# Optimization experiments

Hardware: AMD Instinct MI355X
Metric: run time of the kernel (lower is better)

The kernel has to match this reference:

```python
import jax, jax.numpy as jnp
import numpy as np

K = 8
B = 3.0
DIM = 32
HID = 32
BATCH = 65536
MIN_BW = 1e-3
MIN_BH = 1e-3
MIN_D = 1e-3


def setup_inputs() -> dict:
    key = jax.random.key(0)
    ks = jax.random.split(key, 8)
    L = DIM - 1
    x = jax.random.normal(ks[0], (BATCH, DIM), jnp.float32)
    init_param = jax.random.uniform(ks[1], (3 * K - 1,), jnp.float32, -0.5, 0.5)
    # stacked per-dim FCNN weights; layer l conditions on x[:, :l+1] -> causal zero-mask
    w1 = jax.random.normal(ks[2], (L, L, HID), jnp.float32) * 0.2
    mask = (jnp.arange(L)[None, :] <= jnp.arange(L)[:, None]).astype(jnp.float32)
    w1 = w1 * mask[:, :, None]
    b1 = jax.random.normal(ks[3], (L, HID), jnp.float32) * 0.1
    w2 = jax.random.normal(ks[4], (L, HID, HID), jnp.float32) * 0.2
    b2 = jax.random.normal(ks[5], (L, HID), jnp.float32) * 0.1
    w3 = jax.random.normal(ks[6], (L, HID, 3 * K - 1), jnp.float32) * 0.2
    b3 = jax.random.normal(ks[7], (L, 3 * K - 1), jnp.float32) * 0.1
    return {"x": x, "init_param": init_param, "w1": w1, "b1": b1,
            "w2": w2, "b2": b2, "w3": w3, "b3": b3}


def _rqs_forward(x, Wu, Hu, Du):
    # x: [dim, batch]; Wu, Hu: [dim, batch, K]; Du: [dim, batch, K-1]
    inside = (x >= -B) & (x <= B)
    xc = jnp.clip(x, -B, B)
    # bin widths
    widths = jax.nn.softmax(Wu, axis=-1)
    widths = MIN_BW + (1.0 - MIN_BW * K) * widths
    cw = jnp.cumsum(widths, axis=-1)
    cw = jnp.concatenate([jnp.zeros(cw.shape[:-1] + (1,), cw.dtype), cw], axis=-1)
    cw = 2.0 * B * cw - B
    cw = cw.at[..., 0].set(-B).at[..., -1].set(B)
    widths = cw[..., 1:] - cw[..., :-1]
    # bin heights
    heights = jax.nn.softmax(Hu, axis=-1)
    heights = MIN_BH + (1.0 - MIN_BH * K) * heights
    ch = jnp.cumsum(heights, axis=-1)
    ch = jnp.concatenate([jnp.zeros(ch.shape[:-1] + (1,), ch.dtype), ch], axis=-1)
    ch = 2.0 * B * ch - B
    ch = ch.at[..., 0].set(-B).at[..., -1].set(B)
    heights = ch[..., 1:] - ch[..., :-1]
    # knot derivatives, edges pinned so softplus(const)+min_d = 1
    const = float(np.log(np.exp(1.0 - MIN_D) - 1.0))
    pad = jnp.full(Du.shape[:-1] + (1,), const, Du.dtype)
    derivs = MIN_D + jax.nn.softplus(jnp.concatenate([pad, Du, pad], axis=-1))  # [.., K+1]
    # bin search (searchsorted on cumwidths, eps bump on last edge)
    cw_s = cw.at[..., -1].add(1e-6)
    idx = jnp.sum((xc[..., None] >= cw_s).astype(jnp.int32), axis=-1) - 1
    idx = jnp.clip(idx, 0, K - 1)
    g = lambda a: jnp.take_along_axis(a, idx[..., None], axis=-1)[..., 0]
    in_cw = g(cw)
    in_w = g(widths)
    in_ch = g(ch)
    in_h = g(heights)
    in_delta = g(heights / widths)
    d0 = g(derivs)
    d1 = g(derivs[..., 1:])
    theta = (xc - in_cw) / in_w
    tt = theta * (1.0 - theta)
    num = in_h * (in_delta * theta ** 2 + d0 * tt)
    den = in_delta + (d0 + d1 - 2.0 * in_delta) * tt
    out = in_ch + num / den
    dnum = in_delta ** 2 * (d1 * theta ** 2 + 2.0 * in_delta * tt + d0 * (1.0 - theta) ** 2)
    ld = jnp.log(dnum) - 2.0 * jnp.log(den)
    out = jnp.where(inside, out, x)  # identity tails
    ld = jnp.where(inside, ld, 0.0)
    return out, ld


def reference(x, init_param, w1, b1, w2, b2, w3, b3):
    # all per-dim conditioners at once (w1 is causally masked in setup)
    h1 = jnp.tanh(jnp.einsum('bd,ldh->lbh', x[:, :DIM - 1], w1) + b1[:, None, :])
    h2 = jnp.tanh(jnp.einsum('lbh,lhg->lbg', h1, w2) + b2[:, None, :])
    out = jnp.einsum('lbh,lho->lbo', h2, w3) + b3[:, None, :]  # [dim-1, batch, 3K-1]
    p0 = jnp.broadcast_to(init_param, (1, x.shape[0], 3 * K - 1))
    params = jnp.concatenate([p0, out], axis=0)  # [dim, batch, 3K-1]
    Wu = 2.0 * B * jax.nn.softmax(params[..., :K], axis=-1)
    Hu = 2.0 * B * jax.nn.softmax(params[..., K:2 * K], axis=-1)
    Du = jax.nn.softplus(params[..., 2 * K:])
    z_t, ld = _rqs_forward(x.T, Wu, Hu, Du)  # [dim, batch]
    return z_t.T, jnp.sum(ld, axis=0)
```

## Files before the change

kernel.cpp:

```cpp
#include <hip/hip_runtime.h>
#include <hip/hip_bf16.h>
#include <cmath>

constexpr int KN   = 8;
constexpr int NPAR = 23;
constexpr int DD   = 32;
constexpr float BND   = 3.0f;
constexpr float MINBW = 1e-3f;
constexpr float MIND  = 1e-3f;

#define TPB   256
#define ROWS  256
#define GDIMS 4
#define WST   40
#define PSTH  28
#define RECB  8192

typedef __attribute__((ext_vector_type(8))) short short8;
typedef __attribute__((ext_vector_type(4))) float float4v;
typedef __attribute__((ext_vector_type(2))) __fp16 fp16x2;
typedef __attribute__((ext_vector_type(4))) _Float16 half4v;

#define RCP(x) __builtin_amdgcn_rcpf(x)

__device__ __forceinline__ short f2bf(float f) {
    unsigned u = __float_as_uint(f);
    u += 0x7fffu + ((u >> 16) & 1u);
    return (short)(u >> 16);
}

__device__ __forceinline__ int pkbf(float a, float b) {
    union { __hip_bfloat162 v; int i; } u;
    u.v = __float22bfloat162_rn(make_float2(a, b));
    return u.i;
}

__device__ __forceinline__ int pkh(float a, float b) {
    union { fp16x2 h; int i; } u;
    u.h = __builtin_amdgcn_cvt_pkrtz(a, b);
    return u.i;
}

__device__ __forceinline__ float fast_tanh(float x) {
    float e = __expf(2.0f * x);
    return 1.0f - 2.0f * RCP(e + 1.0f);
}

__device__ __forceinline__ float softplus_fast(float v) {
    return __logf(1.0f + __expf(v));
}

__device__ __forceinline__ float rqs_apply(float xv, const float* p, float& ldout) {
    float cw[KN + 1], ch[KN + 1];
    {
        float t0[KN]; float s = 0.f;
#pragma unroll
        for (int k = 0; k < KN; ++k) { t0[k] = __expf(p[k]); s += t0[k]; }
        float inv = (2.0f * BND) * RCP(s);
        float e2[KN]; float s2 = 0.f;
#pragma unroll
        for (int k = 0; k < KN; ++k) { e2[k] = __expf(inv * t0[k]); s2 += e2[k]; }
        float fac = (1.0f - MINBW * KN) * RCP(s2);
        float c = 0.f;
        cw[0] = -BND;
#pragma unroll
        for (int k = 0; k < KN; ++k) { c += MINBW + fac * e2[k]; cw[k + 1] = 2.0f * BND * c - BND; }
        cw[KN] = BND;
    }
    {
        float t0[KN]; float s = 0.f;
#pragma unroll
        for (int k = 0; k < KN; ++k) { t0[k] = __expf(p[KN + k]); s += t0[k]; }
        float inv = (2.0f * BND) * RCP(s);
        float e2[KN]; float s2 = 0.f;
#pragma unroll
        for (int k = 0; k < KN; ++k) { e2[k] = __expf(inv * t0[k]); s2 += e2[k]; }
        float fac = (1.0f - MINBW * KN) * RCP(s2);
        float c = 0.f;
        ch[0] = -BND;
#pragma unroll
        for (int k = 0; k < KN; ++k) { c += MINBW + fac * e2[k]; ch[k + 1] = 2.0f * BND * c - BND; }
        ch[KN] = BND;
    }

    float xc = fminf(fmaxf(xv, -BND), BND);
    float in_cw = cw[0], in_w = cw[1] - cw[0];
    float in_ch = ch[0], in_h = ch[1] - ch[0];
    float dl0 = 0.0f, dl1 = p[2 * KN];
    bool e0 = true, e1 = false;
#pragma unroll
    for (int k = 1; k < KN; ++k) {
        bool c = (xc >= cw[k]);
        in_cw = c ? cw[k]            : in_cw;
        in_w  = c ? (cw[k+1]-cw[k])  : in_w;
        in_ch = c ? ch[k]            : in_ch;
        in_h  = c ? (ch[k+1]-ch[k])  : in_h;
        dl0   = c ? p[2*KN + k - 1]  : dl0;
        if (k < KN - 1) dl1 = c ? p[2*KN + k] : dl1;
        if (k == 1)      e0 = !c;
        if (k == KN - 1) e1 = c;
    }
    float d0 = e0 ? 1.0f : (MIND + softplus_fast(softplus_fast(dl0)));
    float d1 = e1 ? 1.0f : (MIND + softplus_fast(softplus_fast(dl1)));

    float rw    = RCP(in_w);
    float th    = (xc - in_cw) * rw;
    float delta = in_h * rw;
    float tt    = th * (1.0f - th);
    float th2   = th * th;
    float num   = in_h * (delta * th2 + d0 * tt);
    float den   = delta + (d0 + d1 - 2.0f * delta) * tt;
    float z     = in_ch + num * RCP(den);
    float omt   = 1.0f - th;
    float dnum  = delta * delta * (d1 * th2 + 2.0f * delta * tt + d0 * omt * omt);
    float ldv   = __logf(dnum) - 2.0f * __logf(den);

    bool inside = (xv >= -BND) && (xv <= BND);
    ldout = inside ? ldv : 0.0f;
    return inside ? z : xv;
}

__device__ __forceinline__ short8 xpose_h(float4v cA, float4v cB,
                                          int odd, int sl_a, int sl_b, bool qlow) {
    int a0 = pkbf(fast_tanh(cA[0]), fast_tanh(cA[1]));
    int a1 = pkbf(fast_tanh(cA[2]), fast_tanh(cA[3]));
    int b0 = pkbf(fast_tanh(cB[0]), fast_tanh(cB[1]));
    int b1 = pkbf(fast_tanh(cB[2]), fast_tanh(cB[3]));
    int p0 = odd ? b0 : a0, p1 = odd ? b1 : a1;
    int p2 = odd ? a0 : b0, p3 = odd ? a1 : b1;
    int g0 = __shfl(p0, sl_a, 64);
    int g1 = __shfl(p1, sl_a, 64);
    int g2 = __shfl(p2, sl_b, 64);
    int g3 = __shfl(p3, sl_b, 64);
    union { int4 i; short8 s; } u;
    u.i = qlow ? make_int4(g0, g1, g2, g3) : make_int4(g2, g3, g0, g1);
    return u.s;
}

__device__ __forceinline__ float4v f4v(float4 v) {
    float4v r; r[0] = v.x; r[1] = v.y; r[2] = v.z; r[3] = v.w; return r;
}

struct WFrag {
    short8 w1a, w1b, w2a, w2b, w3a, w3b;
    float4v bA1, bB1, bA2, bB2, bA3, bB3;
};

__device__ __forceinline__ WFrag load_wfrag(const char* __restrict__ wbuf,
                                            int l, int ln, int q) {
    const char* rec = wbuf + (size_t)l * RECB;
    const short* rw = (const short*)rec;
    const float* rb = (const float*)(rec + 7680);
    WFrag f;
    f.w1a = *(const short8*)&rw[ln * WST + q * 8];
    f.w1b = *(const short8*)&rw[(16 + ln) * WST + q * 8];
    f.w2a = *(const short8*)&rw[1280 + ln * WST + q * 8];
    f.w2b = *(const short8*)&rw[1280 + (16 + ln) * WST + q * 8];
    f.w3a = *(const short8*)&rw[2560 + ln * WST + q * 8];
    f.w3b = *(const short8*)&rw[2560 + (16 + ln) * WST + q * 8];
    f.bA1 = f4v(*(const float4*)&rb[4 * q]);
    f.bB1 = f4v(*(const float4*)&rb[16 + 4 * q]);
    f.bA2 = f4v(*(const float4*)&rb[32 + 4 * q]);
    f.bB2 = f4v(*(const float4*)&rb[48 + 4 * q]);
    f.bA3 = f4v(*(const float4*)&rb[64 + 4 * q]);
    f.bB3 = f4v(*(const float4*)&rb[80 + 4 * q]);
    return f;
}

extern "C" __global__ void __launch_bounds__(256)
k_prep(const float* __restrict__ w1, const float* __restrict__ b1,
       const float* __restrict__ w2, const float* __restrict__ b2,
       const float* __restrict__ w3, const float* __restrict__ b3,
       char* __restrict__ wbuf, float* __restrict__ ldo, int B)
{
    const int l = blockIdx.x, tid = threadIdx.x;
    if (l >= 31) {
        const int zb = l - 31;
        const int chunk = B >> 6;
        float4* dst = (float4*)(ldo + (size_t)zb * chunk);
        for (int i = tid; i < (chunk >> 2); i += 256)
            dst[i] = make_float4(0.f, 0.f, 0.f, 0.f);
        return;
    }
    short* r1 = (short*)(wbuf + (size_t)l * RECB);
    short* r2 = r1 + 1280;
    short* r3 = r2 + 1280;
    float* f1 = (float*)(wbuf + (size_t)l * RECB + 7680);
    float* f2 = f1 + 32;
    float* f3 = f2 + 32;
    const float* g1 = w1 + (size_t)l * 992;
    const float* g2 = w2 + (size_t)l * 1024;
    const float* g3 = w3 + (size_t)l * 736;
    for (int i = tid; i < 1280; i += 256) {
        int n = i / WST, k = i - WST * n;
        r1[i] = (k < 31) ? f2bf(g1[k * 32 + n]) : (short)0;
        r2[i] = (k < 32) ? f2bf(g2[k * 32 + n]) : (short)0;
        r3[i] = (n < 23 && k < 32) ? f2bf(g3[k * 23 + n]) : (short)0;
    }
    if (tid < 32) { f1[tid] = b1[(size_t)l * 32 + tid]; f2[tid] = b2[(size_t)l * 32 + tid]; }
    if (tid < 32) f3[tid] = (tid < 23) ? b3[(size_t)l * 23 + tid] : 0.0f;
}

extern "C" __global__ void __launch_bounds__(TPB, 3)
k_nsf(const float* __restrict__ x,
      const float* __restrict__ p0,
      const char* __restrict__ wbuf,
      float* __restrict__ zo, float* __restrict__ ldo, int B)
{
    __shared__ __align__(16) _Float16 sP[ROWS * PSTH];

    const int tid  = threadIdx.x;
    const int lane = tid & 63;
    const int wv   = tid >> 6;
    const int q    = lane >> 4;
    const int ln   = lane & 15;
    const int qb   = q & 1;
    const bool qlow = (q < 2);
    const int s_even = ln + 32 * qb;
    const int s_odd  = s_even + 16;
    const int sl_a = qlow ? s_even : s_odd;
    const int sl_b = qlow ? s_odd  : s_even;
    const int g    = blockIdx.y;
    const int ly0  = GDIMS * g;
    const long long rowbase = (long long)blockIdx.x * ROWS;
    const long long row = rowbase + tid;

    float xarr[GDIMS];
    {
        float4 xs = *(const float4*)(x + row * DD + ly0);
        xarr[0] = xs.x; xarr[1] = xs.y; xarr[2] = xs.z; xarr[3] = xs.w;
    }

    short8 au[4];
#pragma unroll
    for (int t = 0; t < 4; ++t) {
        const int m0 = 64 * wv + 16 * t;
        const float4* xp = (const float4*)(x + (rowbase + m0 + ln) * DD + q * 8);
        float4 uu = xp[0], vv = xp[1];
        union { int4 i; short8 s; } c;
        c.i = make_int4(pkbf(uu.x, uu.y), pkbf(uu.z, uu.w),
                        pkbf(vv.x, vv.y), pkbf(vv.z, vv.w));
        au[t] = c.s;
    }

    float zreg[GDIMS];
    float ldacc = 0.0f;

    WFrag wf = load_wfrag(wbuf, (ly0 == 0) ? 0 : ly0 - 1, ln, q);

#pragma unroll
    for (int j = 0; j < GDIMS; ++j) {
        const int ly = ly0 + j;
        if (ly == 0) {
            float pr[NPAR];
#pragma unroll
            for (int k = 0; k < NPAR; ++k) pr[k] = p0[k];
            float ld;
            zreg[0] = rqs_apply(xarr[0], pr, ld);
            ldacc += ld;
            continue;
        }

        float4v cA[4], cB[4];
#pragma unroll
        for (int t = 0; t < 4; ++t) {
            cA[t] = __builtin_amdgcn_mfma_f32_16x16x32_bf16(wf.w1a, au[t], wf.bA1, 0, 0, 0);
            cB[t] = __builtin_amdgcn_mfma_f32_16x16x32_bf16(wf.w1b, au[t], wf.bB1, 0, 0, 0);
        }
        short8 h1f[4];
#pragma unroll
        for (int t = 0; t < 4; ++t)
            h1f[t] = xpose_h(cA[t], cB[t], qb, sl_a, sl_b, qlow);
#pragma unroll
        for (int t = 0; t < 4; ++t) {
            cA[t] = __builtin_amdgcn_mfma_f32_16x16x32_bf16(wf.w2a, h1f[t], wf.bA2, 0, 0, 0);
            cB[t] = __builtin_amdgcn_mfma_f32_16x16x32_bf16(wf.w2b, h1f[t], wf.bB2, 0, 0, 0);
        }
#pragma unroll
        for (int t = 0; t < 4; ++t)
            h1f[t] = xpose_h(cA[t], cB[t], qb, sl_a, sl_b, qlow);
#pragma unroll
        for (int t = 0; t < 4; ++t) {
            cA[t] = __builtin_amdgcn_mfma_f32_16x16x32_bf16(wf.w3a, h1f[t], wf.bA3, 0, 0, 0);
            cB[t] = __builtin_amdgcn_mfma_f32_16x16x32_bf16(wf.w3b, h1f[t], wf.bB3, 0, 0, 0);
        }
#pragma unroll
        for (int t = 0; t < 4; ++t) {
            const int m0 = 64 * wv + 16 * t;
            int2 pv0 = make_int2(pkh(cA[t][0], cA[t][1]), pkh(cA[t][2], cA[t][3]));
            *(int2*)&sP[(m0 + ln) * PSTH + 4 * q] = pv0;
            if (qlow) {
                int2 pv1 = make_int2(pkh(cB[t][0], cB[t][1]), pkh(cB[t][2], cB[t][3]));
                *(int2*)&sP[(m0 + ln) * PSTH + 16 + 4 * q] = pv1;
            }
        }

        WFrag wfn;
        if (j + 1 < GDIMS) wfn = load_wfrag(wbuf, ly, ln, q);

        {
            const _Float16* pp = &sP[tid * PSTH];
            float pr[24];
#pragma unroll
            for (int u = 0; u < 6; ++u) {
                half4v hv = *(const half4v*)(pp + 4 * u);
                pr[4*u+0] = (float)hv[0];
                pr[4*u+1] = (float)hv[1];
                pr[4*u+2] = (float)hv[2];
                pr[4*u+3] = (float)hv[3];
            }
            float ld;
            zreg[j] = rqs_apply(xarr[j], pr, ld);
            ldacc += ld;
        }
        if (j + 1 < GDIMS) wf = wfn;
    }

    float4 zv = make_float4(zreg[0], zreg[1], zreg[2], zreg[3]);
    *(float4*)(zo + row * DD + ly0) = zv;
    unsafeAtomicAdd(&ldo[row], ldacc);
}

extern "C" void kernel_launch(void* const* d_in, const int* in_sizes, int n_in,
                              void* d_out, int out_size, void* d_ws, size_t ws_size,
                              hipStream_t stream) {
    const float* x  = (const float*)d_in[0];
    const float* p0 = (const float*)d_in[1];
    const float* w1 = (const float*)d_in[2];
    const float* b1 = (const float*)d_in[3];
    const float* w2 = (const float*)d_in[4];
    const float* b2 = (const float*)d_in[5];
    const float* w3 = (const float*)d_in[6];
    const float* b3 = (const float*)d_in[7];

    const int B = in_sizes[0] / DD;
    float* zo  = (float*)d_out;
    float* ldo = zo + (size_t)B * DD;
    char* wbuf = (char*)d_ws;

    hipLaunchKernelGGL(k_prep, dim3(95), dim3(256), 0, stream,
                       w1, b1, w2, b2, w3, b3, wbuf, ldo, B);
    hipLaunchKernelGGL(k_nsf, dim3(B / ROWS, DD / GDIMS), dim3(TPB), 0, stream,
                       x, p0, wbuf, zo, ldo, B);
}
```

Before: 143.4 us.

## Double-buffer spline params in LDS to overlap next MFMA MLP with spline

Splits the per-dimension step into an MFMA conditioner phase that packs spline parameters into one of two LDS buffers, and a spline phase that reads the previous dimension's buffer. Software-pipelines the loop so the GEMMs for dimension j run before the spline for dimension j-1, letting matrix and vector work interleave. Uses explicit lgkmcnt waits instead of barriers, since each thread only reads its own row. Doubles the LDS footprint and lowers the occupancy hint from 3 to 2 blocks per CU to give more registers, at the cost of fewer resident waves for latency hiding.

```diff
diff --git a/kernel.cpp b/kernel.cpp
--- a/kernel.cpp
+++ b/kernel.cpp
@@ -16,10 +16,11 @@
 #define PSTH  28
 #define RECB  8192
 
+#define LGKM_FENCE() asm volatile("s_waitcnt lgkmcnt(0)" ::: "memory")
+
 typedef __attribute__((ext_vector_type(8))) short short8;
 typedef __attribute__((ext_vector_type(4))) float float4v;
 typedef __attribute__((ext_vector_type(2))) __fp16 fp16x2;
-typedef __attribute__((ext_vector_type(4))) _Float16 half4v;
 
 #define RCP(x) __builtin_amdgcn_rcpf(x)
 
@@ -201,13 +202,14 @@
     if (tid < 32) f3[tid] = (tid < 23) ? b3[(size_t)l * 23 + tid] : 0.0f;
 }
 
-extern "C" __global__ void __launch_bounds__(TPB, 3)
+extern "C" __global__ void __launch_bounds__(TPB, 2)
 k_nsf(const float* __restrict__ x,
       const float* __restrict__ p0,
       const char* __restrict__ wbuf,
       float* __restrict__ zo, float* __restrict__ ldo, int B)
 {
-    __shared__ __align__(16) _Float16 sP[ROWS * PSTH];
+    __shared__ __align__(16) _Float16 sPa[ROWS * PSTH];
+    __shared__ __align__(16) _Float16 sPb[ROWS * PSTH];
 
     const int tid  = threadIdx.x;
     const int lane = tid & 63;
@@ -246,75 +248,82 @@
     float zreg[GDIMS];
     float ldacc = 0.0f;
 
-    WFrag wf = load_wfrag(wbuf, (ly0 == 0) ? 0 : ly0 - 1, ln, q);
-
-#pragma unroll
-    for (int j = 0; j < GDIMS; ++j) {
-        const int ly = ly0 + j;
-        if (ly == 0) {
-            float pr[NPAR];
-#pragma unroll
-            for (int k = 0; k < NPAR; ++k) pr[k] = p0[k];
-            float ld;
-            zreg[0] = rqs_apply(xarr[0], pr, ld);
-            ldacc += ld;
-            continue;
-        }
-
+    auto gemm_pack = [&](const WFrag& wf, _Float16* buf) {
         float4v cA[4], cB[4];
 #pragma unroll
         for (int t = 0; t < 4; ++t) {
             cA[t] = __builtin_amdgcn_mfma_f32_16x16x32_bf16(wf.w1a, au[t], wf.bA1, 0, 0, 0);
             cB[t] = __builtin_amdgcn_mfma_f32_16x16x32_bf16(wf.w1b, au[t], wf.bB1, 0, 0, 0);
         }
-        short8 h1f[4];
+        short8 hf[4];
 #pragma unroll
         for (int t = 0; t < 4; ++t)
-            h1f[t] = xpose_h(cA[t], cB[t], qb, sl_a, sl_b, qlow);
+            hf[t] = xpose_h(cA[t], cB[t], qb, sl_a, sl_b, qlow);
 #pragma unroll
         for (int t = 0; t < 4; ++t) {
-            cA[t] = __builtin_amdgcn_mfma_f32_16x16x32_bf16(wf.w2a, h1f[t], wf.bA2, 0, 0, 0);
-            cB[t] = __builtin_amdgcn_mfma_f32_16x16x32_bf16(wf.w2b, h1f[t], wf.bB2, 0, 0, 0);
+            cA[t] = __builtin_amdgcn_mfma_f32_16x16x32_bf16(wf.w2a, hf[t], wf.bA2, 0, 0, 0);
+            cB[t] = __builtin_amdgcn_mfma_f32_16x16x32_bf16(wf.w2b, hf[t], wf.bB2, 0, 0, 0);
         }
 #pragma unroll
         for (int t = 0; t < 4; ++t)
-            h1f[t] = xpose_h(cA[t], cB[t], qb, sl_a, sl_b, qlow);
+            hf[t] = xpose_h(cA[t], cB[t], qb, sl_a, sl_b, qlow);
 #pragma unroll
         for (int t = 0; t < 4; ++t) {
-            cA[t] = __builtin_amdgcn_mfma_f32_16x16x32_bf16(wf.w3a, h1f[t], wf.bA3, 0, 0, 0);
-            cB[t] = __builtin_amdgcn_mfma_f32_16x16x32_bf16(wf.w3b, h1f[t], wf.bB3, 0, 0, 0);
+            cA[t] = __builtin_amdgcn_mfma_f32_16x16x32_bf16(wf.w3a, hf[t], wf.bA3, 0, 0, 0);
+            cB[t] = __builtin_amdgcn_mfma_f32_16x16x32_bf16(wf.w3b, hf[t], wf.bB3, 0, 0, 0);
         }
 #pragma unroll
         for (int t = 0; t < 4; ++t) {
             const int m0 = 64 * wv + 16 * t;
-            int2 pv0 = make_int2(pkh(cA[t][0], cA[t][1]), pkh(cA[t][2], cA[t][3]));
-            *(int2*)&sP[(m0 + ln) * PSTH + 4 * q] = pv0;
-            if (qlow) {
-                int2 pv1 = make_int2(pkh(cB[t][0], cB[t][1]), pkh(cB[t][2], cB[t][3]));
-                *(int2*)&sP[(m0 + ln) * PSTH + 16 + 4 * q] = pv1;
+            int2* prow = (int2*)&buf[(m0 + ln) * PSTH];
+            prow[q] = make_int2(pkh(cA[t][0], cA[t][1]), pkh(cA[t][2], cA[t][3]));
+            if (qlow)
+                prow[4 + q] = make_int2(pkh(cB[t][0], cB[t][1]), pkh(cB[t][2], cB[t][3]));
+        }
+    };
+
+    auto do_spline = [&](const _Float16* buf, int j) {
+        const int2* pp = (const int2*)&buf[tid * PSTH];
+        float pr[24];
+#pragma unroll
+        for (int u = 0; u < 6; ++u) {
+            union { int2 i; _Float16 h[4]; } hv;
+            hv.i = pp[u];
+            pr[4*u+0] = (float)hv.h[0];
+            pr[4*u+1] = (float)hv.h[1];
+            pr[4*u+2] = (float)hv.h[2];
+            pr[4*u+3] = (float)hv.h[3];
+        }
+        float ld;
+        zreg[j] = rqs_apply(xarr[j], pr, ld);
+        ldacc += ld;
+    };
+
+    const int jg = (ly0 == 0) ? 1 : 0;
+    WFrag wf = load_wfrag(wbuf, ly0 + jg - 1, ln, q);
+
+#pragma unroll
+    for (int jj = 0; jj < GDIMS; ++jj) {
+        if (jj < jg) continue;
+        _Float16* buf = (jj & 1) ? sPb : sPa;
+        if (jj > jg) LGKM_FENCE();
+        gemm_pack(wf, buf);
+        if (jj + 1 < GDIMS) wf = load_wfrag(wbuf, ly0 + jj, ln, q);
+        if (jj == jg) {
+            if (ly0 == 0) {
+                float pr[NPAR];
+#pragma unroll
+                for (int k = 0; k < NPAR; ++k) pr[k] = p0[k];
+                float ld;
+                zreg[0] = rqs_apply(xarr[0], pr, ld);
+                ldacc += ld;
             }
-        }
-
-        WFrag wfn;
-        if (j + 1 < GDIMS) wfn = load_wfrag(wbuf, ly, ln, q);
-
-        {
-            const _Float16* pp = &sP[tid * PSTH];
-            float pr[24];
-#pragma unroll
-            for (int u = 0; u < 6; ++u) {
-                half4v hv = *(const half4v*)(pp + 4 * u);
-                pr[4*u+0] = (float)hv[0];
-                pr[4*u+1] = (float)hv[1];
-                pr[4*u+2] = (float)hv[2];
-                pr[4*u+3] = (float)hv[3];
-            }
-            float ld;
-            zreg[j] = rqs_apply(xarr[j], pr, ld);
-            ldacc += ld;
-        }
-        if (j + 1 < GDIMS) wf = wfn;
-    }
+        } else {
+            do_spline(((jj - 1) & 1) ? sPb : sPa, jj - 1);
+        }
+    }
+    LGKM_FENCE();
+    do_spline(((GDIMS - 1) & 1) ? sPb : sPa, GDIMS - 1);
 
     float4 zv = make_float4(zreg[0], zreg[1], zreg[2], zreg[3]);
     *(float4*)(zo + row * DD + ly0) = zv;
```

After: 143.5 us. About the same (+0.1%).
